# Kernel optimization log

Hardware: AMD Instinct MI355X
Metric: run time of the kernel (lower is better)

## Reference

```python
import jax, jax.numpy as jnp
import numpy as np

MAX_ITER = 12   # Taylor order, as in block_expm default
EPS = 1e-7
SQ_CAP = 8      # static cap on scale-square steps (s ~<= 2 for init_scale=0.1 thetas)


def block_expm(A):
    # A: [N, 8, 8] skew-symmetric. Scale-square + Taylor, faithful to the torch code
    # (note: the original squares ALL blocks max_s = max(s) times; we replicate that).
    I = jnp.eye(8, dtype=A.dtype)
    norm = jnp.sqrt(jnp.sum(A * A, axis=(-2, -1), keepdims=True))  # Frobenius
    s = jnp.clip(jnp.ceil(jnp.log2(norm + EPS)), 0.0)              # [N,1,1]
    scale = jnp.power(2.0, s)
    A_scaled = A / (scale + EPS)
    R = jnp.broadcast_to(I, A.shape)
    A_power = A_scaled
    factorial = 1.0
    for i in range(1, MAX_ITER + 1):
        factorial *= i
        R = R + A_power / factorial
        if i < MAX_ITER:
            A_power = jnp.matmul(A_power, A_scaled)
    max_s = jnp.max(s)  # scalar
    for k in range(SQ_CAP):
        R = jnp.where(k < max_s, jnp.matmul(R, R), R)
    return R


def setup_inputs() -> dict:
    key = jax.random.key(0)
    kx, kt = jax.random.split(key)
    B, T, D = 2, 8192, 4096
    num_blocks = D // 8
    x = jax.random.normal(kx, (B, T, D), dtype=jnp.float32)
    theta = jax.random.normal(kt, (num_blocks, 8, 8), dtype=jnp.float32) * 0.1
    return {"x": x, "theta": theta}


def reference(x, theta):
    B, T, D = x.shape
    num_blocks = D // 8
    xv = x.reshape(B, T, num_blocks, 8)
    A = theta - jnp.swapaxes(theta, -1, -2)  # skew-symmetric
    R = block_expm(A)                         # [N, 8, 8]
    y = jnp.einsum('btne,neo->btno', xv, R)
    return y.reshape(B, T, D)
```

## Files before the change

### kernel.cpp

```cpp
#include <hip/hip_runtime.h>
#include <hip/hip_bf16.h>
#include <math.h>


#define MAX_ITER 12
#define EPS 1e-7f
#define SQ_CAP 8
#define ROWS_PER_BLOCK 32

__global__ __launch_bounds__(512) void smax_kernel(const float* __restrict__ theta,
                                                   int* __restrict__ maxs,
                                                   int num_blocks) {
    __shared__ int sm[512];
    int tid = threadIdx.x;
    int s_i = 0;
    if (tid < num_blocks) {
        const float* tb = theta + (size_t)tid * 64;
        float n2 = 0.0f;
        #pragma unroll
        for (int i = 0; i < 8; ++i)
            #pragma unroll
            for (int j = 0; j < 8; ++j) {
                float a = tb[i * 8 + j] - tb[j * 8 + i];
                n2 = fmaf(a, a, n2);
            }
        float norm = sqrtf(n2);
        float s = ceilf(log2f(norm + EPS));
        if (s < 0.0f) s = 0.0f;
        s_i = (int)s;
    }
    sm[tid] = s_i;
    __syncthreads();
    for (int off = 256; off > 0; off >>= 1) {
        if (tid < off && tid + off < 512) sm[tid] = max(sm[tid], sm[tid + off]);
        __syncthreads();
    }
    if (tid == 0) maxs[0] = sm[0];
}

__global__ __launch_bounds__(64) void expm_kernel(const float* __restrict__ theta,
                                                  const int* __restrict__ maxs,
                                                  float* __restrict__ Rbuf) {
    const int n = blockIdx.x;
    const int lane = threadIdx.x;
    const int i = lane >> 3, j = lane & 7;
    const float* tb = theta + (size_t)n * 64;
    float a = tb[i * 8 + j] - tb[j * 8 + i];

    float n2 = a * a;
    #pragma unroll
    for (int off = 32; off >= 1; off >>= 1) n2 += __shfl_xor(n2, off, 64);

    float norm = sqrtf(n2);
    float s = ceilf(log2f(norm + EPS));
    if (s < 0.0f) s = 0.0f;
    float scale = exp2f(s);
    float as = a / (scale + EPS);

    __shared__ float As[64];
    __shared__ float Ap[64];
    As[lane] = as;

    float R = (i == j) ? 1.0f : 0.0f;
    float Apow = as;
    float fact = 1.0f;
    __syncthreads();

    for (int it = 1; it <= MAX_ITER; ++it) {
        fact *= (float)it;
        R += Apow / fact;
        if (it < MAX_ITER) {
            Ap[lane] = Apow;
            __syncthreads();
            float t = 0.0f;
            #pragma unroll
            for (int k = 0; k < 8; ++k) t = fmaf(Ap[i * 8 + k], As[k * 8 + j], t);
            __syncthreads();
            Apow = t;
        }
    }

    int ms = maxs[0];
    if (ms > SQ_CAP) ms = SQ_CAP;
    for (int k2 = 0; k2 < ms; ++k2) {
        Ap[lane] = R;
        __syncthreads();
        float t = 0.0f;
        #pragma unroll
        for (int k = 0; k < 8; ++k) t = fmaf(Ap[i * 8 + k], Ap[k * 8 + j], t);
        __syncthreads();
        R = t;
    }
    Rbuf[(size_t)n * 64 + lane] = R;
}

__global__ __launch_bounds__(256) void apply_kernel(const float* __restrict__ x,
                                                    const float* __restrict__ Rbuf,
                                                    float* __restrict__ y,
                                                    int D) {
    const int tid = threadIdx.x;
    const int n = blockIdx.y * 256 + tid;
    const int r0 = blockIdx.x * ROWS_PER_BLOCK;

    float r[64];
    const float4* Rp = (const float4*)(Rbuf + (size_t)n * 64);
    #pragma unroll
    for (int q = 0; q < 16; ++q) {
        float4 v = Rp[q];
        r[q * 4 + 0] = v.x; r[q * 4 + 1] = v.y;
        r[q * 4 + 2] = v.z; r[q * 4 + 3] = v.w;
    }

    const float* xp = x + (size_t)r0 * D + (size_t)n * 8;
    float*       yp = y + (size_t)r0 * D + (size_t)n * 8;

    #pragma unroll 2
    for (int k = 0; k < ROWS_PER_BLOCK; ++k) {
        float4 x0 = *(const float4*)(xp);
        float4 x1 = *(const float4*)(xp + 4);
        float xe[8] = {x0.x, x0.y, x0.z, x0.w, x1.x, x1.y, x1.z, x1.w};
        float yo[8];
        #pragma unroll
        for (int o = 0; o < 8; ++o) {
            float acc = xe[0] * r[o];
            #pragma unroll
            for (int e = 1; e < 8; ++e) acc = fmaf(xe[e], r[e * 8 + o], acc);
            yo[o] = acc;
        }
        float4 y0 = {yo[0], yo[1], yo[2], yo[3]};
        float4 y1 = {yo[4], yo[5], yo[6], yo[7]};
        *(float4*)(yp)     = y0;
        *(float4*)(yp + 4) = y1;
        xp += D;
        yp += D;
    }
}

extern "C" void kernel_launch(void* const* d_in, const int* in_sizes, int n_in,
                              void* d_out, int out_size, void* d_ws, size_t ws_size,
                              hipStream_t stream) {
    const float* x     = (const float*)d_in[0];
    const float* theta = (const float*)d_in[1];
    float* y = (float*)d_out;

    const int tsize = in_sizes[1];
    const int num_blocks = tsize / 64;
    const int D = num_blocks * 8;
    const long rows = (long)in_sizes[0] / D;

    float* Rbuf = (float*)d_ws;
    int*   maxs = (int*)((char*)d_ws + (size_t)num_blocks * 64 * sizeof(float));

    smax_kernel<<<1, 512, 0, stream>>>(theta, maxs, num_blocks);
    expm_kernel<<<num_blocks, 64, 0, stream>>>(theta, maxs, Rbuf);

    dim3 grid((unsigned)(rows / ROWS_PER_BLOCK), (unsigned)(num_blocks / 256));
    apply_kernel<<<grid, 256, 0, stream>>>(x, Rbuf, y, D);
}
```

Baseline: 460.2 us.

## Fold max-scale reduction into expm kernel and split apply rows across lane pairs

Removes the separate single-block smax kernel: every expm block now redundantly scans all theta blocks to compute the global max squaring count, saving a launch at the cost of repeated theta reads. The apply kernel now assigns each 8-wide block to two threads, each loading one float4 of x and exchanging the other half via lane shuffles. This gives fully coalesced contiguous float4 accesses and halves per-thread register use for R (32 floats instead of 64), which is meant to raise occupancy and memory efficiency in the bandwidth-bound apply pass.

```diff
diff --git a/kernel.cpp b/kernel.cpp
--- a/kernel.cpp
+++ b/kernel.cpp
@@ -1,5 +1,4 @@
 #include <hip/hip_runtime.h>
-#include <hip/hip_bf16.h>
 #include <math.h>
 
 
@@ -8,44 +7,44 @@
 #define SQ_CAP 8
 #define ROWS_PER_BLOCK 32
 
-__global__ __launch_bounds__(512) void smax_kernel(const float* __restrict__ theta,
-                                                   int* __restrict__ maxs,
-                                                   int num_blocks) {
-    __shared__ int sm[512];
-    int tid = threadIdx.x;
-    int s_i = 0;
-    if (tid < num_blocks) {
-        const float* tb = theta + (size_t)tid * 64;
-        float n2 = 0.0f;
-        #pragma unroll
-        for (int i = 0; i < 8; ++i)
-            #pragma unroll
-            for (int j = 0; j < 8; ++j) {
-                float a = tb[i * 8 + j] - tb[j * 8 + i];
-                n2 = fmaf(a, a, n2);
-            }
-        float norm = sqrtf(n2);
-        float s = ceilf(log2f(norm + EPS));
-        if (s < 0.0f) s = 0.0f;
-        s_i = (int)s;
-    }
-    sm[tid] = s_i;
-    __syncthreads();
-    for (int off = 256; off > 0; off >>= 1) {
-        if (tid < off && tid + off < 512) sm[tid] = max(sm[tid], sm[tid + off]);
-        __syncthreads();
-    }
-    if (tid == 0) maxs[0] = sm[0];
-}
-
 __global__ __launch_bounds__(64) void expm_kernel(const float* __restrict__ theta,
-                                                  const int* __restrict__ maxs,
-                                                  float* __restrict__ Rbuf) {
+                                                  float* __restrict__ Rbuf,
+                                                  int num_blocks) {
     const int n = blockIdx.x;
     const int lane = threadIdx.x;
     const int i = lane >> 3, j = lane & 7;
-    const float* tb = theta + (size_t)n * 64;
-    float a = tb[i * 8 + j] - tb[j * 8 + i];
+
+    float maxn2 = 0.0f;
+    for (int b = lane; b < num_blocks; b += 64) {
+        const float4* tp = (const float4*)(theta + (size_t)b * 64);
+        float t[64];
+        #pragma unroll
+        for (int q = 0; q < 16; ++q) {
+            float4 v = tp[q];
+            t[q * 4 + 0] = v.x; t[q * 4 + 1] = v.y;
+            t[q * 4 + 2] = v.z; t[q * 4 + 3] = v.w;
+        }
+        float n2b = 0.0f;
+        #pragma unroll
+        for (int ii = 0; ii < 8; ++ii)
+            #pragma unroll
+            for (int jj = 0; jj < 8; ++jj) {
+                float d = t[ii * 8 + jj] - t[jj * 8 + ii];
+                n2b = fmaf(d, d, n2b);
+            }
+        maxn2 = fmaxf(maxn2, n2b);
+    }
+    #pragma unroll
+    for (int off = 32; off >= 1; off >>= 1)
+        maxn2 = fmaxf(maxn2, __shfl_xor(maxn2, off, 64));
+    float smax = ceilf(log2f(sqrtf(maxn2) + EPS));
+    if (smax < 0.0f) smax = 0.0f;
+    int ms = (int)smax;
+    if (ms > SQ_CAP) ms = SQ_CAP;
+
+    float e = theta[(size_t)n * 64 + lane];
+    float eT = __shfl(e, ((lane & 7) << 3) | (lane >> 3), 64);
+    float a = e - eT;
 
     float n2 = a * a;
     #pragma unroll
@@ -80,8 +79,6 @@
         }
     }
 
-    int ms = maxs[0];
-    if (ms > SQ_CAP) ms = SQ_CAP;
     for (int k2 = 0; k2 < ms; ++k2) {
         Ap[lane] = R;
         __syncthreads();
@@ -99,40 +96,47 @@
                                                     float* __restrict__ y,
                                                     int D) {
     const int tid = threadIdx.x;
-    const int n = blockIdx.y * 256 + tid;
-    const int r0 = blockIdx.x * ROWS_PER_BLOCK;
+    const int f = blockIdx.y * 256 + tid;
+    const int n = f >> 1;
+    const int h = f & 1;
+    const long r0 = (long)blockIdx.x * ROWS_PER_BLOCK;
 
-    float r[64];
-    const float4* Rp = (const float4*)(Rbuf + (size_t)n * 64);
+    float4 rr[8];
+    const float* Rb = Rbuf + (size_t)n * 64 + h * 4;
     #pragma unroll
-    for (int q = 0; q < 16; ++q) {
-        float4 v = Rp[q];
-        r[q * 4 + 0] = v.x; r[q * 4 + 1] = v.y;
-        r[q * 4 + 2] = v.z; r[q * 4 + 3] = v.w;
+    for (int k = 0; k < 8; ++k) {
+        int e = (k < 4) ? (h * 4 + k) : ((1 - h) * 4 + (k - 4));
+        rr[k] = *(const float4*)(Rb + e * 8);
     }
 
-    const float* xp = x + (size_t)r0 * D + (size_t)n * 8;
-    float*       yp = y + (size_t)r0 * D + (size_t)n * 8;
+    const int d4 = D >> 2;
+    const float4* xp = (const float4*)(x + r0 * D) + f;
+    float4*       yp = (float4*)(y + r0 * D) + f;
 
-    #pragma unroll 2
+    #pragma unroll 4
     for (int k = 0; k < ROWS_PER_BLOCK; ++k) {
-        float4 x0 = *(const float4*)(xp);
-        float4 x1 = *(const float4*)(xp + 4);
-        float xe[8] = {x0.x, x0.y, x0.z, x0.w, x1.x, x1.y, x1.z, x1.w};
-        float yo[8];
+        float4 v = *xp;
+        float4 u;
+        u.x = __shfl_xor(v.x, 1, 64);
+        u.y = __shfl_xor(v.y, 1, 64);
+        u.z = __shfl_xor(v.z, 1, 64);
+        u.w = __shfl_xor(v.w, 1, 64);
+        float xv[8] = {v.x, v.y, v.z, v.w, u.x, u.y, u.z, u.w};
+        float4 acc;
+        acc.x = xv[0] * rr[0].x;
+        acc.y = xv[0] * rr[0].y;
+        acc.z = xv[0] * rr[0].z;
+        acc.w = xv[0] * rr[0].w;
         #pragma unroll
-        for (int o = 0; o < 8; ++o) {
-            float acc = xe[0] * r[o];
-            #pragma unroll
-            for (int e = 1; e < 8; ++e) acc = fmaf(xe[e], r[e * 8 + o], acc);
-            yo[o] = acc;
+        for (int k2 = 1; k2 < 8; ++k2) {
+            acc.x = fmaf(xv[k2], rr[k2].x, acc.x);
+            acc.y = fmaf(xv[k2], rr[k2].y, acc.y);
+            acc.z = fmaf(xv[k2], rr[k2].z, acc.z);
+            acc.w = fmaf(xv[k2], rr[k2].w, acc.w);
         }
-        float4 y0 = {yo[0], yo[1], yo[2], yo[3]};
-        float4 y1 = {yo[4], yo[5], yo[6], yo[7]};
-        *(float4*)(yp)     = y0;
-        *(float4*)(yp + 4) = y1;
-        xp += D;
-        yp += D;
+        *yp = acc;
+        xp += d4;
+        yp += d4;
     }
 }
 
@@ -149,11 +153,9 @@
     const long rows = (long)in_sizes[0] / D;
 
     float* Rbuf = (float*)d_ws;
-    int*   maxs = (int*)((char*)d_ws + (size_t)num_blocks * 64 * sizeof(float));
 
-    smax_kernel<<<1, 512, 0, stream>>>(theta, maxs, num_blocks);
-    expm_kernel<<<num_blocks, 64, 0, stream>>>(theta, maxs, Rbuf);
+    expm_kernel<<<num_blocks, 64, 0, stream>>>(theta, Rbuf, num_blocks);
 
-    dim3 grid((unsigned)(rows / ROWS_PER_BLOCK), (unsigned)(num_blocks / 256));
+    dim3 grid((unsigned)(rows / ROWS_PER_BLOCK), (unsigned)(D / 1024));
     apply_kernel<<<grid, 256, 0, stream>>>(x, Rbuf, y, D);
 }
```

Result: no change. 465.3 us (+1.1%).
